# Kernel tuning notes

Measured on AMD Instinct MI355X. Metric: run time of the kernel, lower is better.

Reference implementation:

```python
import jax, jax.numpy as jnp
import numpy as np

B, T, NU, NX, NY = 16, 4096, 64, 256, 32

def setup_inputs() -> dict:
    key = jax.random.key(0)
    ks = jax.random.split(key, 7)
    s = 1.0 / np.sqrt(NX)
    return {
        "inputs": jax.random.normal(ks[0], (B, T, NU), dtype=jnp.float32),
        "h0": jax.random.uniform(ks[1], (B, NX), dtype=jnp.float32),
        "H_w": jax.random.normal(ks[2], (NX, NX), dtype=jnp.float32) * s,
        "H_b": jax.random.normal(ks[3], (NX,), dtype=jnp.float32) * s,
        "K_w": jax.random.normal(ks[4], (NX, NU), dtype=jnp.float32) * (1.0 / np.sqrt(NU)),
        "E_inv": jnp.eye(NX, dtype=jnp.float32),  # E = I in the original module
        "out_w": jax.random.normal(ks[5], (NY, NX), dtype=jnp.float32) * s,
        "out_b": jax.random.normal(ks[6], (NY,), dtype=jnp.float32) * s,
    }

def reference(inputs, h0, H_w, H_b, K_w, E_inv, out_w, out_b):
    # Precompute input projections for all steps: [B, T, NX]
    Ku = jnp.einsum("btu,xu->btx", inputs, K_w)
    seq_len = inputs.shape[1]

    def step(ht, ku_t):
        xt = ht @ H_w.T + H_b + ku_t          # Linear(H) + Linear(K)
        ht_new = jax.nn.relu(xt) @ E_inv      # nonlinearity then fixed matrix
        return ht_new, ht_new

    # loop runs seq_len - 1 times; states start with h0
    _, hs = jax.lax.scan(step, h0, jnp.swapaxes(Ku[:, : seq_len - 1, :], 0, 1))
    states = jnp.concatenate([h0[:, None, :], jnp.swapaxes(hs, 0, 1)], axis=1)  # [B, T, NX]
    yest = states @ out_w.T + out_b  # [B, T, NY]
    return (yest, states)
```

## Files before the change

### kernel.cpp

```cpp
#include <hip/hip_runtime.h>

#define Bsz 16
#define Tl  4096
#define NUc 64
#define NXc 256
#define NYc 32

template <int CTRL>
__device__ __forceinline__ float dpp_add(float x) {
    int y = __builtin_amdgcn_update_dpp(0, __float_as_int(x), CTRL, 0xf, 0xf, true);
    return x + __int_as_float(y);
}
__device__ __forceinline__ float reduce8(float x) {
    x = dpp_add<0xB1>(x);
    x = dpp_add<0x4E>(x);
    x = dpp_add<0x141>(x);
    return x;
}
__device__ __forceinline__ float row_reduce16(float x) {
    x = dpp_add<0x128>(x);
    x = dpp_add<0x124>(x);
    x = dpp_add<0x4E>(x);
    x = dpp_add<0xB1>(x);
    return x;
}

__device__ __forceinline__ void fast_barrier() {
    asm volatile("s_waitcnt lgkmcnt(0)\n\ts_barrier" ::: "memory");
}

#define KEEPF(x) asm volatile("" : "+v"(x))

#define DECLW(T,P) \
    float T##P##_0,T##P##_1,T##P##_2,T##P##_3,T##P##_4,T##P##_5,T##P##_6,T##P##_7, \
          T##P##_8,T##P##_9,T##P##_10,T##P##_11,T##P##_12,T##P##_13,T##P##_14,T##P##_15
#define LOADW(T,P,RP) { \
    const float* wr_ = (RP) + 16*P; \
    float4 a_=*(const float4*)(wr_+0), b_=*(const float4*)(wr_+4); \
    float4 c_=*(const float4*)(wr_+8), d_=*(const float4*)(wr_+12); \
    T##P##_0 =a_.x; T##P##_1 =a_.y; T##P##_2 =a_.z; T##P##_3 =a_.w; \
    T##P##_4 =b_.x; T##P##_5 =b_.y; T##P##_6 =b_.z; T##P##_7 =b_.w; \
    T##P##_8 =c_.x; T##P##_9 =c_.y; T##P##_10=c_.z; T##P##_11=c_.w; \
    T##P##_12=d_.x; T##P##_13=d_.y; T##P##_14=d_.z; T##P##_15=d_.w; }
#define PINW(T,P) \
    KEEPF(T##P##_0);  KEEPF(T##P##_1);  KEEPF(T##P##_2);  KEEPF(T##P##_3);  \
    KEEPF(T##P##_4);  KEEPF(T##P##_5);  KEEPF(T##P##_6);  KEEPF(T##P##_7);  \
    KEEPF(T##P##_8);  KEEPF(T##P##_9);  KEEPF(T##P##_10); KEEPF(T##P##_11); \
    KEEPF(T##P##_12); KEEPF(T##P##_13); KEEPF(T##P##_14); KEEPF(T##P##_15)
#define FMAW(T,P,AC0,AC1) \
    AC0=fmaf(T##P##_0, hv0, AC0); AC1=fmaf(T##P##_1, hv1, AC1); \
    AC0=fmaf(T##P##_2, hv2, AC0); AC1=fmaf(T##P##_3, hv3, AC1); \
    AC0=fmaf(T##P##_4, hv4, AC0); AC1=fmaf(T##P##_5, hv5, AC1); \
    AC0=fmaf(T##P##_6, hv6, AC0); AC1=fmaf(T##P##_7, hv7, AC1); \
    AC0=fmaf(T##P##_8, hv8, AC0); AC1=fmaf(T##P##_9, hv9, AC1); \
    AC0=fmaf(T##P##_10,hv10,AC0); AC1=fmaf(T##P##_11,hv11,AC1); \
    AC0=fmaf(T##P##_12,hv12,AC0); AC1=fmaf(T##P##_13,hv13,AC1); \
    AC0=fmaf(T##P##_14,hv14,AC0); AC1=fmaf(T##P##_15,hv15,AC1)

#define CHUNK4(P, O0, O1, O2, O3) { \
    float4 q0_ = *(const float4*)(rb + O0); \
    float4 q1_ = *(const float4*)(rb + O1); \
    float4 q2_ = *(const float4*)(rb + O2); \
    float4 q3_ = *(const float4*)(rb + O3); \
    float hv0=q0_.x, hv1=q0_.y, hv2 =q0_.z, hv3 =q0_.w; \
    float hv4=q1_.x, hv5=q1_.y, hv6 =q1_.z, hv7 =q1_.w; \
    float hv8=q2_.x, hv9=q2_.y, hv10=q2_.z, hv11=q2_.w; \
    float hv12=q3_.x,hv13=q3_.y,hv14=q3_.z, hv15=q3_.w; \
    FMAW(A,P,aA0,aA1); FMAW(B,P,aB0,aB1); \
    FMAW(C,P,aC0,aC1); FMAW(D,P,aD0,aD1); }

#define DECLK8(T) float kk##T##_0,kk##T##_1,kk##T##_2,kk##T##_3,kk##T##_4,kk##T##_5,kk##T##_6,kk##T##_7
#define LOADK8(T,RP) { \
    float4 a_=*(const float4*)(RP), b_=*(const float4*)((RP)+4); \
    kk##T##_0=a_.x; kk##T##_1=a_.y; kk##T##_2=a_.z; kk##T##_3=a_.w; \
    kk##T##_4=b_.x; kk##T##_5=b_.y; kk##T##_6=b_.z; kk##T##_7=b_.w; }
#define PINK8(T) \
    KEEPF(kk##T##_0); KEEPF(kk##T##_1); KEEPF(kk##T##_2); KEEPF(kk##T##_3); \
    KEEPF(kk##T##_4); KEEPF(kk##T##_5); KEEPF(kk##T##_6); KEEPF(kk##T##_7)
#define FMAK8(T,AC0,AC1) \
    AC0=fmaf(kk##T##_0,uu0,AC0); AC1=fmaf(kk##T##_1,uu1,AC1); \
    AC0=fmaf(kk##T##_2,uu2,AC0); AC1=fmaf(kk##T##_3,uu3,AC1); \
    AC0=fmaf(kk##T##_4,uu4,AC0); AC1=fmaf(kk##T##_5,uu5,AC1); \
    AC0=fmaf(kk##T##_6,uu6,AC0); AC1=fmaf(kk##T##_7,uu7,AC1)

#define KDECL4(Q)  float k##Q##_0, k##Q##_1, k##Q##_2, k##Q##_3
#define KLOAD4(Q) { float4 v_ = *(const float4*)(wr_ + 4*Q); \
    k##Q##_0 = v_.x; k##Q##_1 = v_.y; k##Q##_2 = v_.z; k##Q##_3 = v_.w; }
#define KPIN4(Q)   KEEPF(k##Q##_0); KEEPF(k##Q##_1); KEEPF(k##Q##_2); KEEPF(k##Q##_3)
#define KACC4(Q, U) { \
    s0_ = fmaf(k##Q##_0, (U).x, s0_); s1_ = fmaf(k##Q##_1, (U).y, s1_); \
    s0_ = fmaf(k##Q##_2, (U).z, s0_); s1_ = fmaf(k##Q##_3, (U).w, s1_); }

__global__ __launch_bounds__(256) void ku_kernel(const float* __restrict__ inputs,
                                                 const float* __restrict__ Kw,
                                                 float* __restrict__ Ku) {
    const int x    = threadIdx.x;
    const int row0 = blockIdx.x * 64;

    const float* wr_ = Kw + (size_t)x * NUc;
    KDECL4(0);  KDECL4(1);  KDECL4(2);  KDECL4(3);
    KDECL4(4);  KDECL4(5);  KDECL4(6);  KDECL4(7);
    KDECL4(8);  KDECL4(9);  KDECL4(10); KDECL4(11);
    KDECL4(12); KDECL4(13); KDECL4(14); KDECL4(15);
    KLOAD4(0);  KLOAD4(1);  KLOAD4(2);  KLOAD4(3);
    KLOAD4(4);  KLOAD4(5);  KLOAD4(6);  KLOAD4(7);
    KLOAD4(8);  KLOAD4(9);  KLOAD4(10); KLOAD4(11);
    KLOAD4(12); KLOAD4(13); KLOAD4(14); KLOAD4(15);
    KPIN4(0);  KPIN4(1);  KPIN4(2);  KPIN4(3);
    KPIN4(4);  KPIN4(5);  KPIN4(6);  KPIN4(7);
    KPIN4(8);  KPIN4(9);  KPIN4(10); KPIN4(11);
    KPIN4(12); KPIN4(13); KPIN4(14); KPIN4(15);

    __shared__ float sin_[64 * NUc];
    {
        const float* src = inputs + (size_t)row0 * NUc;
        #pragma unroll
        for (int i = 0; i < 16; ++i)
            sin_[threadIdx.x + i * 256] = src[threadIdx.x + i * 256];
    }
    __syncthreads();

    for (int r = 0; r < 64; ++r) {
        const float4* hp = (const float4*)(&sin_[r * NUc]);
        float s0_ = 0.f, s1_ = 0.f;
        KACC4(0,  hp[0]);  KACC4(1,  hp[1]);  KACC4(2,  hp[2]);  KACC4(3,  hp[3]);
        KACC4(4,  hp[4]);  KACC4(5,  hp[5]);  KACC4(6,  hp[6]);  KACC4(7,  hp[7]);
        KACC4(8,  hp[8]);  KACC4(9,  hp[9]);  KACC4(10, hp[10]); KACC4(11, hp[11]);
        KACC4(12, hp[12]); KACC4(13, hp[13]); KACC4(14, hp[14]); KACC4(15, hp[15]);
        Ku[(size_t)(row0 + r) * NXc + x] = s0_ + s1_;
    }
}

template <bool USE_KU>
__global__ __attribute__((amdgpu_flat_work_group_size(512, 512),
                          amdgpu_waves_per_eu(2, 2)))
void scan4(const float* __restrict__ Ku,
           const float* __restrict__ inputs,
           const float* __restrict__ Kw,
           const float* __restrict__ h0,
           const float* __restrict__ Hw,
           const float* __restrict__ Hb,
           float* __restrict__ states) {
    const int b   = blockIdx.x;
    const int tid = threadIdx.x;
    const int c   = tid & 7;
    const int jg  = tid >> 3;
    const int r0  = 4 * jg;
    const int row_w = r0 + (c & 3);

    __shared__ __align__(16) char shmem[4096];
    float* shf = (float*)shmem;

    DECLW(A,0); DECLW(A,1); DECLW(B,0); DECLW(B,1);
    DECLW(C,0); DECLW(C,1); DECLW(D,0); DECLW(D,1);
    {
        const float* p = Hw + (size_t)r0 * NXc + 32 * c;
        LOADW(A,0,p); LOADW(A,1,p);  p += NXc;
        LOADW(B,0,p); LOADW(B,1,p);  p += NXc;
        LOADW(C,0,p); LOADW(C,1,p);  p += NXc;
        LOADW(D,0,p); LOADW(D,1,p);
    }
    DECLK8(A); DECLK8(B); DECLK8(C); DECLK8(D);
    if (!USE_KU) {
        const float* q = Kw + (size_t)r0 * NUc + 8 * c;
        LOADK8(A,q); q += NUc; LOADK8(B,q); q += NUc;
        LOADK8(C,q); q += NUc; LOADK8(D,q);
    }

    const float bias = Hb[row_w];

    const int wr_pos = row_w + 4 * (row_w >> 5);
    int wr_off = 2048 + 4 * wr_pos;
    int rd_off = 144 * c;

    const float* kub = Ku + (size_t)b * Tl * NXc;
    const float* inb = inputs + (size_t)b * Tl * NUc + 8 * c;
    float*       stb = states + (size_t)b * Tl * NXc;

    float kuv = 0.f;
    float uu0,uu1,uu2,uu3,uu4,uu5,uu6,uu7;
    if (USE_KU) {
        kuv = kub[row_w];
    } else {
        float4 a_ = *(const float4*)(inb + 0), b_ = *(const float4*)(inb + 4);
        uu0=a_.x; uu1=a_.y; uu2=a_.z; uu3=a_.w;
        uu4=b_.x; uu5=b_.y; uu6=b_.z; uu7=b_.w;
    }

    int st_idx = row_w;
    {
        float h = h0[b * NXc + row_w];
        shf[wr_pos] = h;
        stb[st_idx] = h;
    }
    __syncthreads();

    for (int t = 0; t < Tl - 1; ++t) {
        PINW(A,0); PINW(A,1); PINW(B,0); PINW(B,1);
        PINW(C,0); PINW(C,1); PINW(D,0); PINW(D,1);
        if (!USE_KU) { PINK8(A); PINK8(B); PINK8(C); PINK8(D); }

        const char* rb = (const char*)shmem + rd_off;

        float ku_nxt = 0.f;
        float4 un0, un1;
        if (USE_KU) {
            ku_nxt = kub[(size_t)(t + 1) * NXc + row_w];
        } else {
            int tn = t + 1; if (tn > Tl - 2) tn = Tl - 2;
            const float* up = inb + (size_t)tn * NUc;
            un0 = *(const float4*)(up + 0); un1 = *(const float4*)(up + 4);
        }

        float aA0=0.f,aA1=0.f,aB0=0.f,aB1=0.f,aC0=0.f,aC1=0.f,aD0=0.f,aD1=0.f;
        CHUNK4(0,  0, 16, 32, 48);
        CHUNK4(1, 64, 80, 96, 112);
        if (!USE_KU) {
            FMAK8(A,aA0,aA1); FMAK8(B,aB0,aB1);
            FMAK8(C,aC0,aC1); FMAK8(D,aD0,aD1);
        }

        float sA = reduce8(aA0 + aA1);
        float sB = reduce8(aB0 + aB1);
        float sC = reduce8(aC0 + aC1);
        float sD = reduce8(aD0 + aD1);

        float x = (c & 1) ? sB : sA;
        float y = (c & 1) ? sD : sC;
        float v = (c & 2) ? y : x;
        float s = v + bias + (USE_KU ? kuv : 0.f);
        float h = s > 0.f ? s : 0.f;

        *(float*)((char*)shmem + wr_off) = h;
        st_idx += NXc;
        stb[st_idx] = h;

        if (USE_KU) {
            kuv = ku_nxt;
        } else {
            uu0=un0.x; uu1=un0.y; uu2=un0.z; uu3=un0.w;
            uu4=un1.x; uu5=un1.y; uu6=un1.z; uu7=un1.w;
        }
        fast_barrier();
        rd_off ^= 2048;
        wr_off ^= 2048;
    }
}

__global__ __launch_bounds__(512, 2) void yest2(const float* __restrict__ states,
                                                const float* __restrict__ ow,
                                                const float* __restrict__ obv,
                                                float* __restrict__ yest) {
    const int tid = threadIdx.x;
    const int c   = tid & 15;
    const int g   = tid >> 4;

    float y0_,y1_,y2_,y3_,y4_,y5_,y6_,y7_,y8_,y9_,y10_,y11_,y12_,y13_,y14_,y15_;
    {
        const float* wr = ow + (size_t)g * NXc + 16 * c;
        float4 vA = *(const float4*)(wr + 0),  vB = *(const float4*)(wr + 4);
        float4 vC = *(const float4*)(wr + 8),  vD = *(const float4*)(wr + 12);
        y0_=vA.x; y1_=vA.y; y2_ =vA.z; y3_ =vA.w;
        y4_=vB.x; y5_=vB.y; y6_ =vB.z; y7_ =vB.w;
        y8_=vC.x; y9_=vC.y; y10_=vC.z; y11_=vC.w;
        y12_=vD.x;y13_=vD.y;y14_=vD.z; y15_=vD.w;
        KEEPF(y0_); KEEPF(y1_); KEEPF(y2_);  KEEPF(y3_);
        KEEPF(y4_); KEEPF(y5_); KEEPF(y6_);  KEEPF(y7_);
        KEEPF(y8_); KEEPF(y9_); KEEPF(y10_); KEEPF(y11_);
        KEEPF(y12_);KEEPF(y13_);KEEPF(y14_); KEEPF(y15_);
    }
    const float ob = obv[g];

    const int row0 = blockIdx.x * 128;
    for (int r = 0; r < 128; r += 2) {
        const float* s0p = states + (size_t)(row0 + r) * NXc + 16 * c;
        const float* s1p = s0p + NXc;
        float4 A0 = *(const float4*)(s0p + 0), A1 = *(const float4*)(s0p + 4);
        float4 A2 = *(const float4*)(s0p + 8), A3 = *(const float4*)(s0p + 12);
        float4 B0 = *(const float4*)(s1p + 0), B1 = *(const float4*)(s1p + 4);
        float4 B2 = *(const float4*)(s1p + 8), B3 = *(const float4*)(s1p + 12);
        float acc0 = y0_*A0.x + y1_*A0.y + y2_*A0.z + y3_*A0.w
                   + y4_*A1.x + y5_*A1.y + y6_*A1.z + y7_*A1.w
                   + y8_*A2.x + y9_*A2.y + y10_*A2.z + y11_*A2.w
                   + y12_*A3.x + y13_*A3.y + y14_*A3.z + y15_*A3.w;
        float acc1 = y0_*B0.x + y1_*B0.y + y2_*B0.z + y3_*B0.w
                   + y4_*B1.x + y5_*B1.y + y6_*B1.z + y7_*B1.w
                   + y8_*B2.x + y9_*B2.y + y10_*B2.z + y11_*B2.w
                   + y12_*B3.x + y13_*B3.y + y14_*B3.z + y15_*B3.w;
        acc0 = row_reduce16(acc0);
        acc1 = row_reduce16(acc1);
        if (c == 0) {
            yest[(size_t)(row0 + r)     * NYc + g] = acc0 + ob;
            yest[(size_t)(row0 + r + 1) * NYc + g] = acc1 + ob;
        }
    }
}

extern "C" void kernel_launch(void* const* d_in, const int* in_sizes, int n_in,
                              void* d_out, int out_size, void* d_ws, size_t ws_size,
                              hipStream_t stream) {
    const float* inputs = (const float*)d_in[0];
    const float* h0     = (const float*)d_in[1];
    const float* Hw     = (const float*)d_in[2];
    const float* Hb     = (const float*)d_in[3];
    const float* Kw     = (const float*)d_in[4];
    const float* ow     = (const float*)d_in[6];
    const float* ob     = (const float*)d_in[7];

    float* yest   = (float*)d_out;
    float* states = (float*)d_out + (size_t)Bsz * Tl * NYc;

    const size_t ku_bytes = (size_t)Bsz * Tl * NXc * sizeof(float);
    const int    nrows    = Bsz * Tl;

    if (ws_size >= ku_bytes) {
        float* Ku = (float*)d_ws;
        ku_kernel<<<dim3(nrows / 64), dim3(256), 0, stream>>>(inputs, Kw, Ku);
        scan4<true><<<dim3(Bsz), dim3(512), 0, stream>>>(Ku, inputs, Kw, h0, Hw, Hb, states);
    } else {
        scan4<false><<<dim3(Bsz), dim3(512), 0, stream>>>(nullptr, inputs, Kw, h0, Hw, Hb, states);
    }
    yest2<<<dim3(nrows / 128), dim3(512), 0, stream>>>(states, ow, ob, yest);
}
```

Before: 2.055 ms.

## Precompute wave-local hidden-state chunk before barrier in recurrent scan

Weights are now split into eight 4-column chunks per row, permuted per wave so each wave's first chunk covers the hidden units that wave itself writes. After writing h, each wave waits only for its own LDS writes and folds that chunk into the next step's accumulators before the block-wide barrier. This takes one eighth of the matvec off the post-barrier critical path. It also interleaves the four DPP reductions for ILP and unrolls the loop by two so the double-buffer offsets are constants, at the cost of more complex indexing and register pressure.

```diff
diff --git a/kernel.cpp b/kernel.cpp
--- a/kernel.cpp
+++ b/kernel.cpp
@@ -10,12 +10,6 @@
 __device__ __forceinline__ float dpp_add(float x) {
     int y = __builtin_amdgcn_update_dpp(0, __float_as_int(x), CTRL, 0xf, 0xf, true);
     return x + __int_as_float(y);
-}
-__device__ __forceinline__ float reduce8(float x) {
-    x = dpp_add<0xB1>(x);
-    x = dpp_add<0x4E>(x);
-    x = dpp_add<0x141>(x);
-    return x;
 }
 __device__ __forceinline__ float row_reduce16(float x) {
     x = dpp_add<0x128>(x);
@@ -25,49 +19,31 @@
     return x;
 }
 
-__device__ __forceinline__ void fast_barrier() {
-    asm volatile("s_waitcnt lgkmcnt(0)\n\ts_barrier" ::: "memory");
-}
-
 #define KEEPF(x) asm volatile("" : "+v"(x))
 
-#define DECLW(T,P) \
-    float T##P##_0,T##P##_1,T##P##_2,T##P##_3,T##P##_4,T##P##_5,T##P##_6,T##P##_7, \
-          T##P##_8,T##P##_9,T##P##_10,T##P##_11,T##P##_12,T##P##_13,T##P##_14,T##P##_15
-#define LOADW(T,P,RP) { \
-    const float* wr_ = (RP) + 16*P; \
-    float4 a_=*(const float4*)(wr_+0), b_=*(const float4*)(wr_+4); \
-    float4 c_=*(const float4*)(wr_+8), d_=*(const float4*)(wr_+12); \
-    T##P##_0 =a_.x; T##P##_1 =a_.y; T##P##_2 =a_.z; T##P##_3 =a_.w; \
-    T##P##_4 =b_.x; T##P##_5 =b_.y; T##P##_6 =b_.z; T##P##_7 =b_.w; \
-    T##P##_8 =c_.x; T##P##_9 =c_.y; T##P##_10=c_.z; T##P##_11=c_.w; \
-    T##P##_12=d_.x; T##P##_13=d_.y; T##P##_14=d_.z; T##P##_15=d_.w; }
-#define PINW(T,P) \
-    KEEPF(T##P##_0);  KEEPF(T##P##_1);  KEEPF(T##P##_2);  KEEPF(T##P##_3);  \
-    KEEPF(T##P##_4);  KEEPF(T##P##_5);  KEEPF(T##P##_6);  KEEPF(T##P##_7);  \
-    KEEPF(T##P##_8);  KEEPF(T##P##_9);  KEEPF(T##P##_10); KEEPF(T##P##_11); \
-    KEEPF(T##P##_12); KEEPF(T##P##_13); KEEPF(T##P##_14); KEEPF(T##P##_15)
-#define FMAW(T,P,AC0,AC1) \
-    AC0=fmaf(T##P##_0, hv0, AC0); AC1=fmaf(T##P##_1, hv1, AC1); \
-    AC0=fmaf(T##P##_2, hv2, AC0); AC1=fmaf(T##P##_3, hv3, AC1); \
-    AC0=fmaf(T##P##_4, hv4, AC0); AC1=fmaf(T##P##_5, hv5, AC1); \
-    AC0=fmaf(T##P##_6, hv6, AC0); AC1=fmaf(T##P##_7, hv7, AC1); \
-    AC0=fmaf(T##P##_8, hv8, AC0); AC1=fmaf(T##P##_9, hv9, AC1); \
-    AC0=fmaf(T##P##_10,hv10,AC0); AC1=fmaf(T##P##_11,hv11,AC1); \
-    AC0=fmaf(T##P##_12,hv12,AC0); AC1=fmaf(T##P##_13,hv13,AC1); \
-    AC0=fmaf(T##P##_14,hv14,AC0); AC1=fmaf(T##P##_15,hv15,AC1)
-
-#define CHUNK4(P, O0, O1, O2, O3) { \
-    float4 q0_ = *(const float4*)(rb + O0); \
-    float4 q1_ = *(const float4*)(rb + O1); \
-    float4 q2_ = *(const float4*)(rb + O2); \
-    float4 q3_ = *(const float4*)(rb + O3); \
-    float hv0=q0_.x, hv1=q0_.y, hv2 =q0_.z, hv3 =q0_.w; \
-    float hv4=q1_.x, hv5=q1_.y, hv6 =q1_.z, hv7 =q1_.w; \
-    float hv8=q2_.x, hv9=q2_.y, hv10=q2_.z, hv11=q2_.w; \
-    float hv12=q3_.x,hv13=q3_.y,hv14=q3_.z, hv15=q3_.w; \
-    FMAW(A,P,aA0,aA1); FMAW(B,P,aB0,aB1); \
-    FMAW(C,P,aC0,aC1); FMAW(D,P,aD0,aD1); }
+#define DECLC(T,J) float W##T##J##_0, W##T##J##_1, W##T##J##_2, W##T##J##_3
+#define LOADC(T,J,P) { float4 v_ = *(const float4*)(P); \
+    W##T##J##_0=v_.x; W##T##J##_1=v_.y; W##T##J##_2=v_.z; W##T##J##_3=v_.w; }
+#define PINC(T,J) KEEPF(W##T##J##_0); KEEPF(W##T##J##_1); \
+                  KEEPF(W##T##J##_2); KEEPF(W##T##J##_3)
+#define FMAC(T,J,Q,AC) \
+    AC=fmaf(W##T##J##_0,(Q).x,AC); AC=fmaf(W##T##J##_1,(Q).y,AC); \
+    AC=fmaf(W##T##J##_2,(Q).z,AC); AC=fmaf(W##T##J##_3,(Q).w,AC)
+
+#define DECLROW(T) DECLC(T,0); DECLC(T,1); DECLC(T,2); DECLC(T,3); \
+                   DECLC(T,4); DECLC(T,5); DECLC(T,6); DECLC(T,7)
+#define LOADROW(T,BASE) \
+    LOADC(T,0,(BASE)+4*p0); LOADC(T,1,(BASE)+4*p1); \
+    LOADC(T,2,(BASE)+4*p2); LOADC(T,3,(BASE)+4*p3); \
+    LOADC(T,4,(BASE)+4*p4); LOADC(T,5,(BASE)+4*p5); \
+    LOADC(T,6,(BASE)+4*p6); LOADC(T,7,(BASE)+4*p7)
+#define PINROW(T) PINC(T,0); PINC(T,1); PINC(T,2); PINC(T,3); \
+                  PINC(T,4); PINC(T,5); PINC(T,6); PINC(T,7)
+#define FMAROW(T,A0,A1) \
+    FMAC(T,1,Q1,A1); FMAC(T,2,Q2,A0); FMAC(T,3,Q3,A1); FMAC(T,4,Q4,A0); \
+    FMAC(T,5,Q5,A1); FMAC(T,6,Q6,A0); FMAC(T,7,Q7,A1)
+#define CARRY4(T,Q) c##T = fmaf(W##T##0_3,(Q).w, fmaf(W##T##0_2,(Q).z, \
+                     fmaf(W##T##0_1,(Q).y, W##T##0_0*(Q).x)))
 
 #define DECLK8(T) float kk##T##_0,kk##T##_1,kk##T##_2,kk##T##_3,kk##T##_4,kk##T##_5,kk##T##_6,kk##T##_7
 #define LOADK8(T,RP) { \
@@ -78,10 +54,10 @@
     KEEPF(kk##T##_0); KEEPF(kk##T##_1); KEEPF(kk##T##_2); KEEPF(kk##T##_3); \
     KEEPF(kk##T##_4); KEEPF(kk##T##_5); KEEPF(kk##T##_6); KEEPF(kk##T##_7)
 #define FMAK8(T,AC0,AC1) \
-    AC0=fmaf(kk##T##_0,uu0,AC0); AC1=fmaf(kk##T##_1,uu1,AC1); \
-    AC0=fmaf(kk##T##_2,uu2,AC0); AC1=fmaf(kk##T##_3,uu3,AC1); \
-    AC0=fmaf(kk##T##_4,uu4,AC0); AC1=fmaf(kk##T##_5,uu5,AC1); \
-    AC0=fmaf(kk##T##_6,uu6,AC0); AC1=fmaf(kk##T##_7,uu7,AC1)
+    AC0=fmaf(kk##T##_0,uu0.x,AC0); AC1=fmaf(kk##T##_1,uu0.y,AC1); \
+    AC0=fmaf(kk##T##_2,uu0.z,AC0); AC1=fmaf(kk##T##_3,uu0.w,AC1); \
+    AC0=fmaf(kk##T##_4,uu1.x,AC0); AC1=fmaf(kk##T##_5,uu1.y,AC1); \
+    AC0=fmaf(kk##T##_6,uu1.z,AC0); AC1=fmaf(kk##T##_7,uu1.w,AC1)
 
 #define KDECL4(Q)  float k##Q##_0, k##Q##_1, k##Q##_2, k##Q##_3
 #define KLOAD4(Q) { float4 v_ = *(const float4*)(wr_ + 4*Q); \
@@ -134,7 +110,7 @@
 template <bool USE_KU>
 __global__ __attribute__((amdgpu_flat_work_group_size(512, 512),
                           amdgpu_waves_per_eu(2, 2)))
-void scan4(const float* __restrict__ Ku,
+void scan5(const float* __restrict__ Ku,
            const float* __restrict__ inputs,
            const float* __restrict__ Kw,
            const float* __restrict__ h0,
@@ -145,22 +121,35 @@
     const int tid = threadIdx.x;
     const int c   = tid & 7;
     const int jg  = tid >> 3;
+    const int w   = tid >> 6;
     const int r0  = 4 * jg;
     const int row_w = r0 + (c & 3);
 
     __shared__ __align__(16) char shmem[4096];
-    float* shf = (float*)shmem;
-
-    DECLW(A,0); DECLW(A,1); DECLW(B,0); DECLW(B,1);
-    DECLW(C,0); DECLW(C,1); DECLW(D,0); DECLW(D,1);
+    char* shm = shmem;
+
+    const int base8 = 8 * w + c;
+    const int p0 = base8,            p1 = (base8 +  8) & 63;
+    const int p2 = (base8 + 16) & 63, p3 = (base8 + 24) & 63;
+    const int p4 = (base8 + 32) & 63, p5 = (base8 + 40) & 63;
+    const int p6 = (base8 + 48) & 63, p7 = (base8 + 56) & 63;
+    int voff0 = 16 * (p0 + (p0 >> 3)), voff1 = 16 * (p1 + (p1 >> 3));
+    int voff2 = 16 * (p2 + (p2 >> 3)), voff3 = 16 * (p3 + (p3 >> 3));
+    int voff4 = 16 * (p4 + (p4 >> 3)), voff5 = 16 * (p5 + (p5 >> 3));
+    int voff6 = 16 * (p6 + (p6 >> 3)), voff7 = 16 * (p7 + (p7 >> 3));
+    KEEPF(voff0); KEEPF(voff1); KEEPF(voff2); KEEPF(voff3);
+    KEEPF(voff4); KEEPF(voff5); KEEPF(voff6); KEEPF(voff7);
+
+    DECLROW(A); DECLROW(B); DECLROW(C); DECLROW(D);
     {
-        const float* p = Hw + (size_t)r0 * NXc + 32 * c;
-        LOADW(A,0,p); LOADW(A,1,p);  p += NXc;
-        LOADW(B,0,p); LOADW(B,1,p);  p += NXc;
-        LOADW(C,0,p); LOADW(C,1,p);  p += NXc;
-        LOADW(D,0,p); LOADW(D,1,p);
+        const float* pA = Hw + (size_t)(r0 + 0) * NXc;
+        const float* pB = Hw + (size_t)(r0 + 1) * NXc;
+        const float* pC = Hw + (size_t)(r0 + 2) * NXc;
+        const float* pD = Hw + (size_t)(r0 + 3) * NXc;
+        LOADROW(A, pA); LOADROW(B, pB); LOADROW(C, pC); LOADROW(D, pD);
     }
     DECLK8(A); DECLK8(B); DECLK8(C); DECLK8(D);
+    const float* uptr = inputs + (size_t)b * Tl * NUc + 8 * c;
     if (!USE_KU) {
         const float* q = Kw + (size_t)r0 * NUc + 8 * c;
         LOADK8(A,q); q += NUc; LOADK8(B,q); q += NUc;
@@ -168,83 +157,74 @@
     }
 
     const float bias = Hb[row_w];
-
-    const int wr_pos = row_w + 4 * (row_w >> 5);
-    int wr_off = 2048 + 4 * wr_pos;
-    int rd_off = 144 * c;
-
-    const float* kub = Ku + (size_t)b * Tl * NXc;
-    const float* inb = inputs + (size_t)b * Tl * NUc + 8 * c;
-    float*       stb = states + (size_t)b * Tl * NXc;
-
-    float kuv = 0.f;
-    float uu0,uu1,uu2,uu3,uu4,uu5,uu6,uu7;
-    if (USE_KU) {
-        kuv = kub[row_w];
-    } else {
-        float4 a_ = *(const float4*)(inb + 0), b_ = *(const float4*)(inb + 4);
-        uu0=a_.x; uu1=a_.y; uu2=a_.z; uu3=a_.w;
-        uu4=b_.x; uu5=b_.y; uu6=b_.z; uu7=b_.w;
-    }
-
-    int st_idx = row_w;
+    const int wbyte  = 4 * (row_w + 4 * (row_w >> 5));
+
+    const float* kup = Ku + (size_t)b * Tl * NXc + NXc + row_w;
+    float*       stp = states + (size_t)b * Tl * NXc + NXc + row_w;
+
+    float cA, cB, cC, cD;
+    float bk;
     {
         float h = h0[b * NXc + row_w];
-        shf[wr_pos] = h;
-        stb[st_idx] = h;
-    }
-    __syncthreads();
-
-    for (int t = 0; t < Tl - 1; ++t) {
-        PINW(A,0); PINW(A,1); PINW(B,0); PINW(B,1);
-        PINW(C,0); PINW(C,1); PINW(D,0); PINW(D,1);
-        if (!USE_KU) { PINK8(A); PINK8(B); PINK8(C); PINK8(D); }
-
-        const char* rb = (const char*)shmem + rd_off;
-
-        float ku_nxt = 0.f;
-        float4 un0, un1;
+        states[(size_t)b * Tl * NXc + row_w] = h;
+        *(float*)(shm + wbyte) = h;
         if (USE_KU) {
-            ku_nxt = kub[(size_t)(t + 1) * NXc + row_w];
+            bk = bias + Ku[(size_t)b * Tl * NXc + row_w];
         } else {
-            int tn = t + 1; if (tn > Tl - 2) tn = Tl - 2;
-            const float* up = inb + (size_t)tn * NUc;
-            un0 = *(const float4*)(up + 0); un1 = *(const float4*)(up + 4);
+            bk = bias;
         }
-
-        float aA0=0.f,aA1=0.f,aB0=0.f,aB1=0.f,aC0=0.f,aC1=0.f,aD0=0.f,aD1=0.f;
-        CHUNK4(0,  0, 16, 32, 48);
-        CHUNK4(1, 64, 80, 96, 112);
-        if (!USE_KU) {
-            FMAK8(A,aA0,aA1); FMAK8(B,aB0,aB1);
-            FMAK8(C,aC0,aC1); FMAK8(D,aD0,aD1);
-        }
-
-        float sA = reduce8(aA0 + aA1);
-        float sB = reduce8(aB0 + aB1);
-        float sC = reduce8(aC0 + aC1);
-        float sD = reduce8(aD0 + aD1);
-
-        float x = (c & 1) ? sB : sA;
-        float y = (c & 1) ? sD : sC;
-        float v = (c & 2) ? y : x;
-        float s = v + bias + (USE_KU ? kuv : 0.f);
-        float h = s > 0.f ? s : 0.f;
-
-        *(float*)((char*)shmem + wr_off) = h;
-        st_idx += NXc;
-        stb[st_idx] = h;
-
-        if (USE_KU) {
-            kuv = ku_nxt;
-        } else {
-            uu0=un0.x; uu1=un0.y; uu2=un0.z; uu3=un0.w;
-            uu4=un1.x; uu5=un1.y; uu6=un1.z; uu7=un1.w;
-        }
-        fast_barrier();
-        rd_off ^= 2048;
-        wr_off ^= 2048;
-    }
+        asm volatile("s_waitcnt lgkmcnt(0)" ::: "memory");
+        float4 Q0_ = *(const float4*)(shm + voff0);
+        CARRY4(A, Q0_); CARRY4(B, Q0_); CARRY4(C, Q0_); CARRY4(D, Q0_);
+        __syncthreads();
+    }
+
+#define STEPBODY(RD, WR) { \
+    PINROW(A); PINROW(B); PINROW(C); PINROW(D); \
+    if (!USE_KU) { PINK8(A); PINK8(B); PINK8(C); PINK8(D); } \
+    float4 Q1 = *(const float4*)(shm + voff1 + (RD)); \
+    float4 Q2 = *(const float4*)(shm + voff2 + (RD)); \
+    float4 Q3 = *(const float4*)(shm + voff3 + (RD)); \
+    float4 Q4 = *(const float4*)(shm + voff4 + (RD)); \
+    float4 Q5 = *(const float4*)(shm + voff5 + (RD)); \
+    float4 Q6 = *(const float4*)(shm + voff6 + (RD)); \
+    float4 Q7 = *(const float4*)(shm + voff7 + (RD)); \
+    float kn_ = 0.f; float4 uu0, uu1; \
+    if (USE_KU) { kn_ = *kup; kup += NXc; } \
+    else { uu0 = *(const float4*)uptr; uu1 = *(const float4*)(uptr + 4); uptr += NUc; } \
+    float aA0 = cA, aA1 = 0.f, aB0 = cB, aB1 = 0.f; \
+    float aC0 = cC, aC1 = 0.f, aD0 = cD, aD1 = 0.f; \
+    FMAROW(A, aA0, aA1); FMAROW(B, aB0, aB1); \
+    FMAROW(C, aC0, aC1); FMAROW(D, aD0, aD1); \
+    if (!USE_KU) { FMAK8(A,aA0,aA1); FMAK8(B,aB0,aB1); \
+                   FMAK8(C,aC0,aC1); FMAK8(D,aD0,aD1); } \
+    float rA = aA0 + aA1, rB = aB0 + aB1, rC = aC0 + aC1, rD = aD0 + aD1; \
+    rA = dpp_add<0xB1>(rA); rB = dpp_add<0xB1>(rB); \
+    rC = dpp_add<0xB1>(rC); rD = dpp_add<0xB1>(rD); \
+    rA = dpp_add<0x4E>(rA); rB = dpp_add<0x4E>(rB); \
+    rC = dpp_add<0x4E>(rC); rD = dpp_add<0x4E>(rD); \
+    rA = dpp_add<0x141>(rA); rB = dpp_add<0x141>(rB); \
+    rC = dpp_add<0x141>(rC); rD = dpp_add<0x141>(rD); \
+    float x_ = (c & 1) ? rB : rA; \
+    float y_ = (c & 1) ? rD : rC; \
+    float v_ = (c & 2) ? y_ : x_; \
+    float s_ = v_ + bk; \
+    float h_ = s_ > 0.f ? s_ : 0.f; \
+    *stp = h_; stp += NXc; \
+    *(float*)(shm + wbyte + (WR)) = h_; \
+    asm volatile("s_waitcnt lgkmcnt(0)" ::: "memory"); \
+    float4 Q0_ = *(const float4*)(shm + voff0 + (WR)); \
+    CARRY4(A, Q0_); CARRY4(B, Q0_); CARRY4(C, Q0_); CARRY4(D, Q0_); \
+    bk = USE_KU ? (bias + kn_) : bias; \
+    asm volatile("s_waitcnt lgkmcnt(0)\n\ts_barrier" ::: "memory"); \
+}
+
+    for (int tt = 0; tt < (Tl - 2) / 2; ++tt) {
+        STEPBODY(0, 2048);
+        STEPBODY(2048, 0);
+    }
+    STEPBODY(0, 2048);
+#undef STEPBODY
 }
 
 __global__ __launch_bounds__(512, 2) void yest2(const float* __restrict__ states,
@@ -316,9 +296,9 @@
     if (ws_size >= ku_bytes) {
         float* Ku = (float*)d_ws;
         ku_kernel<<<dim3(nrows / 64), dim3(256), 0, stream>>>(inputs, Kw, Ku);
-        scan4<true><<<dim3(Bsz), dim3(512), 0, stream>>>(Ku, inputs, Kw, h0, Hw, Hb, states);
+        scan5<true><<<dim3(Bsz), dim3(512), 0, stream>>>(Ku, inputs, Kw, h0, Hw, Hb, states);
     } else {
-        scan4<false><<<dim3(Bsz), dim3(512), 0, stream>>>(nullptr, inputs, Kw, h0, Hw, Hb, states);
+        scan5<false><<<dim3(Bsz), dim3(512), 0, stream>>>(nullptr, inputs, Kw, h0, Hw, Hb, states);
     }
     yest2<<<dim3(nrows / 128), dim3(512), 0, stream>>>(states, ow, ob, yest);
 }
```

Result: slower. 2.464 ms (+19.9%).
